# Performance work log

Hardware: AMD Instinct MI355X
Metric: run time of the kernel (lower is better)

Reference implementation:

```python
import jax, jax.numpy as jnp
import numpy as np

B = 65536
DIM = 256       # latent_dim
N_EMBED = 1024  # codebook size


def setup_inputs() -> dict:
    key = jax.random.key(0)
    kx, ke = jax.random.split(key)
    x = jax.random.normal(kx, (B, DIM), dtype=jnp.float32)
    # rosinality Quantize stores codebook as embed[dim, n_embed]
    embed = jax.random.normal(ke, (DIM, N_EMBED), dtype=jnp.float32)
    return {"x": x, "embed": embed}


def reference(x, embed):
    # dist[b, k] = ||x_b||^2 - 2 x_b . e_k + ||e_k||^2  (negated for argmax in
    # the original; equivalent to argmin of the distance)
    x_sq = jnp.sum(x * x, axis=1, keepdims=True)            # [B, 1]
    e_sq = jnp.sum(embed * embed, axis=0, keepdims=True)    # [1, K]
    dist = x_sq - 2.0 * (x @ embed) + e_sq                  # [B, K]
    embed_ind = jnp.argmin(dist, axis=1)                    # [B] int
    # codebook lookup: embed.T is [K, dim]
    quantize = jnp.take(embed.T, embed_ind, axis=0)         # [B, dim]
    # commitment loss term
    diff = jnp.mean(jnp.square(jax.lax.stop_gradient(quantize) - x))
    # straight-through estimator
    quantize_st = x + jax.lax.stop_gradient(quantize - x)
    return quantize_st, diff, embed_ind
```

## Files before the change

### kernel.cpp

```cpp
#include <hip/hip_runtime.h>

#define NROWSQ   65536
#define NDIM     256
#define NCB      1024
#define DIFF_OFF 16777216
#define IDX_OFF  16777217

#define MARGIN_A 0.35f
#define MARGIN_B 1.5e-3f
#define SCORE_SHIFT 384.0f

typedef __attribute__((ext_vector_type(8))) short s16x8;
typedef __attribute__((ext_vector_type(4))) float f32x4;

__device__ __forceinline__ unsigned short f2bf(float f) {
  union { float f; unsigned u; } v; v.f = f;
  return (unsigned short)((v.u + 0x7FFFu + ((v.u >> 16) & 1u)) >> 16);
}

__device__ __forceinline__ void gll16(const void* g, void* l) {
  __builtin_amdgcn_global_load_lds(
      (const __attribute__((address_space(1))) unsigned int*)g,
      (__attribute__((address_space(3))) unsigned int*)l, 16, 0, 0);
}

__device__ __forceinline__ void top2_update(float& v1, int& i1, float& v2, int& i2,
                                            float v, int col) {
  if (v > v1 || (v == v1 && col < i1)) { v2 = v1; i2 = i1; v1 = v; i1 = col; }
  else if (v > v2 || (v == v2 && col < i2)) { v2 = v; i2 = col; }
}
__device__ __forceinline__ void top2_merge(float& v1, int& i1, float& v2, int& i2,
                                           float ov1, int oi1, float ov2, int oi2) {
  if (ov1 > v1 || (ov1 == v1 && oi1 < i1)) {
    float nv2 = v1; int ni2 = i1;
    if (ov2 > nv2 || (ov2 == nv2 && oi2 < ni2)) { nv2 = ov2; ni2 = oi2; }
    v1 = ov1; i1 = oi1; v2 = nv2; i2 = ni2;
  } else if (ov1 > v2 || (ov1 == v2 && oi1 < i2)) {
    v2 = ov1; i2 = oi1;
  }
}

__device__ __forceinline__ float np_pairwise128(const float* p) {
  float r0 = p[0], r1 = p[1], r2 = p[2], r3 = p[3];
  float r4 = p[4], r5 = p[5], r6 = p[6], r7 = p[7];
  for (int i = 8; i < 128; i += 8) {
    r0 += p[i];     r1 += p[i + 1]; r2 += p[i + 2]; r3 += p[i + 3];
    r4 += p[i + 4]; r5 += p[i + 5]; r6 += p[i + 6]; r7 += p[i + 7];
  }
  return ((r0 + r1) + (r2 + r3)) + ((r4 + r5) + (r6 + r7));
}

__global__ void k0a_transpose(const float* __restrict__ E, float* __restrict__ embT,
                              unsigned short* __restrict__ cbT,
                              int* __restrict__ cntA, int* __restrict__ cntB) {
  __shared__ float T[64][65];
  const int t = threadIdx.x;
  const int kbase = (blockIdx.x & 15) * 64;
  const int dbase = (blockIdx.x >> 4) * 64;
  if (blockIdx.x == 0 && t == 0) { *cntA = 0; *cntB = 0; }
  #pragma unroll
  for (int i = 0; i < 4; ++i) {
    const int cid = i * 256 + t;
    const int dl = cid >> 4, kc = cid & 15;
    const float4 v = *(const float4*)(E + (size_t)(dbase + dl) * NCB + kbase + kc * 4);
    T[dl][kc * 4 + 0] = v.x; T[dl][kc * 4 + 1] = v.y;
    T[dl][kc * 4 + 2] = v.z; T[dl][kc * 4 + 3] = v.w;
  }
  __syncthreads();
  #pragma unroll
  for (int i = 0; i < 4; ++i) {
    const int cid = i * 256 + t;
    const int kl = cid >> 4, dc = cid & 15;
    float4 v;
    v.x = T[dc * 4 + 0][kl]; v.y = T[dc * 4 + 1][kl];
    v.z = T[dc * 4 + 2][kl]; v.w = T[dc * 4 + 3][kl];
    *(float4*)(embT + (size_t)(kbase + kl) * NDIM + dbase + dc * 4) = v;
    ushort4 b;
    b.x = f2bf(v.x); b.y = f2bf(v.y); b.z = f2bf(v.z); b.w = f2bf(v.w);
    const int dcol = dbase + dc * 4;
    const int sp = dcol ^ ((kl & 7) << 3);
    *(ushort4*)(cbT + (size_t)(kbase + kl) * NDIM + sp) = b;
  }
}

__global__ void k0b_esq(const float* __restrict__ embT, float* __restrict__ esq32,
                        float* __restrict__ esqs, float* __restrict__ esqr) {
  const int b = blockIdx.x, t = threadIdx.x;
  if (b < 128) {
    const int col = b * 8 + (t >> 5);
    const int l = t & 31;
    double s = 0.0;
    #pragma unroll
    for (int i = 0; i < 8; ++i) {
      const double v = (double)embT[(size_t)col * NDIM + l + i * 32];
      s += v * v;
    }
    #pragma unroll
    for (int m = 16; m >= 1; m >>= 1) s += __shfl_xor(s, m);
    if (l == 0) {
      esq32[col] = (float)(0.5 * s);
      esqs[col] = (float)(0.5 * s) - SCORE_SHIFT;
    }
  } else {
    __shared__ float Ls[16][260];
    const int col0 = (b - 128) * 16;
    #pragma unroll
    for (int i = 0; i < 4; ++i) {
      const int flat = i * 256 + t;
      const int row = flat >> 6, f4 = flat & 63;
      *(float4*)&Ls[row][f4 * 4] =
          *(const float4*)(embT + (size_t)(col0 + row) * NDIM + f4 * 4);
    }
    __syncthreads();
    if (t < 16) {
      float sr = 0.f;
      for (int d = 0; d < NDIM; ++d) {
        const float v = Ls[t][d];
        sr = sr + v * v;
      }
      esqr[col0 + t] = sr;
    }
  }
}

__global__ void k1_scores(
    const float* __restrict__ X, const unsigned short* __restrict__ cbT,
    const float* __restrict__ esqs, int2* __restrict__ part1) {
  __shared__ __align__(16) unsigned short Bs[2][64 * 256];
  __shared__ float esq_l[1024];
  const int t = threadIdx.x;
  const int lane = t & 63, w = t >> 6;
  const int l15 = lane & 15, quad = lane >> 4;
  const int rowbase = blockIdx.x * 128;
  const int swz = (l15 & 7) << 3;

  #pragma unroll
  for (int i = 0; i < 8; ++i)
    gll16(cbT + (size_t)(i * 256 + t) * 8, &Bs[0][(i * 256 + w * 64) * 8]);

  s16x8 afrag[2][8];
  #pragma unroll
  for (int m = 0; m < 2; ++m) {
    const float* xr = X + (size_t)(rowbase + w * 32 + m * 16 + l15) * NDIM;
    #pragma unroll
    for (int ks = 0; ks < 8; ++ks) {
      const float4 xa = *(const float4*)(xr + ks * 32 + quad * 8);
      const float4 xb = *(const float4*)(xr + ks * 32 + quad * 8 + 4);
      s16x8 a;
      a[0] = (short)f2bf(xa.x); a[1] = (short)f2bf(xa.y);
      a[2] = (short)f2bf(xa.z); a[3] = (short)f2bf(xa.w);
      a[4] = (short)f2bf(xb.x); a[5] = (short)f2bf(xb.y);
      a[6] = (short)f2bf(xb.z); a[7] = (short)f2bf(xb.w);
      afrag[m][ks] = a;
    }
  }

  {
    const float4 e4 = *(const float4*)(esqs + t * 4);
    *(float4*)(esq_l + t * 4) = e4;
  }

  int key1[2][4], key2[2][4];
  #pragma unroll
  for (int m = 0; m < 2; ++m)
    #pragma unroll
    for (int r = 0; r < 4; ++r) { key1[m][r] = 0; key2[m][r] = 0; }

  asm volatile("s_waitcnt vmcnt(0)" ::: "memory");
  __syncthreads();

  int cur = 0;
  for (int nt = 0; nt < 16; ++nt) {
    if (nt < 15) {
      const unsigned short* src = cbT + (size_t)(nt + 1) * (64 * 256);
      #pragma unroll
      for (int i = 0; i < 8; ++i)
        gll16(src + (size_t)(i * 256 + t) * 8, &Bs[cur ^ 1][(i * 256 + w * 64) * 8]);
    }

    f32x4 acc[2][4];
    #pragma unroll
    for (int m = 0; m < 2; ++m)
      #pragma unroll
      for (int s = 0; s < 4; ++s) acc[m][s] = (f32x4){0.f, 0.f, 0.f, 0.f};

    #pragma unroll
    for (int ks = 0; ks < 8; ++ks) {
      #pragma unroll
      for (int s = 0; s < 4; ++s) {
        const int us = (s * 16 + l15) * 256 + ((ks * 32 + quad * 8) ^ swz);
        const s16x8 bfr = *(const s16x8*)&Bs[cur][us];
        acc[0][s] = __builtin_amdgcn_mfma_f32_16x16x32_bf16(afrag[0][ks], bfr, acc[0][s], 0, 0, 0);
        acc[1][s] = __builtin_amdgcn_mfma_f32_16x16x32_bf16(afrag[1][ks], bfr, acc[1][s], 0, 0, 0);
      }
    }

    #pragma unroll
    for (int s = 0; s < 4; ++s) {
      const int lcol = nt * 64 + s * 16 + l15;
      const float eq = esq_l[lcol];
      const int suffix = 1023 - lcol;
      #pragma unroll
      for (int m = 0; m < 2; ++m)
        #pragma unroll
        for (int r = 0; r < 4; ++r) {
          float sc = acc[m][s][r] - eq;
          sc = fmaxf(sc, 1.0f);
          const int key = (__float_as_int(sc) & 0xFFFFFC00) | suffix;
          key2[m][r] = max(key2[m][r], min(key1[m][r], key));
          key1[m][r] = max(key1[m][r], key);
        }
    }

    asm volatile("s_waitcnt vmcnt(0)" ::: "memory");
    __syncthreads();
    cur ^= 1;
  }

  #pragma unroll
  for (int mask = 1; mask <= 8; mask <<= 1) {
    #pragma unroll
    for (int m = 0; m < 2; ++m)
      #pragma unroll
      for (int r = 0; r < 4; ++r) {
        const int ok1 = __shfl_xor(key1[m][r], mask);
        const int ok2 = __shfl_xor(key2[m][r], mask);
        const int n1 = max(key1[m][r], ok1);
        const int n2 = max(min(key1[m][r], ok1), max(key2[m][r], ok2));
        key1[m][r] = n1; key2[m][r] = n2;
      }
  }

  if (l15 == 0) {
    #pragma unroll
    for (int m = 0; m < 2; ++m)
      #pragma unroll
      for (int r = 0; r < 4; ++r) {
        const int grow = rowbase + w * 32 + m * 16 + quad * 4 + r;
        part1[grow] = make_int2(key1[m][r], key2[m][r]);
      }
  }
}

__global__ void k1m_merge(const int2* __restrict__ part1, float* __restrict__ outIdx,
                          int* __restrict__ cntA, int* __restrict__ listA,
                          float* __restrict__ outDiff) {
  const int row = blockIdx.x * 256 + threadIdx.x;
  if (row == 0) *outDiff = 0.f;
  const int2 a = part1[row];
  outIdx[row] = (float)(1023 - (a.x & 1023));
  const float g1 = __int_as_float(a.x & 0xFFFFFC00);
  const float g2 = __int_as_float(a.y & 0xFFFFFC00);
  if (g1 - g2 < MARGIN_A) {
    const int p = atomicAdd(cntA, 1);
    listA[p] = row;
  }
}

__global__ __launch_bounds__(256) void k2a_refine(
    const float* __restrict__ X, const float* __restrict__ E,
    const float* __restrict__ esq, const int* __restrict__ cntA,
    const int* __restrict__ listA, float4* __restrict__ part2) {
  __shared__ float Xs[8][NDIM];
  __shared__ float rv1[4][8], rv2[4][8];
  __shared__ int   ri1[4][8], ri2[4][8];
  const int t = threadIdx.x;
  const int lane = t & 63, w = t >> 6;
  const int half = blockIdx.x & 1;
  const int bstride = gridDim.x >> 1;
  const int cnt = *cntA;
  const int k0 = half * 512 + t * 2;
  for (int base = (blockIdx.x >> 1) * 8; base < cnt; base += bstride * 8) {
    const int nrows = min(8, cnt - base);
    __syncthreads();
    for (int r = 0; r < 8; ++r) {
      const int rid = listA[base + min(r, nrows - 1)];
      Xs[r][t] = X[(size_t)rid * NDIM + t];
    }
    __syncthreads();

    float acc[8][2];
    #pragma unroll
    for (int r = 0; r < 8; ++r) { acc[r][0] = 0.f; acc[r][1] = 0.f; }

    for (int d = 0; d < NDIM; ++d) {
      const float2 e = *(const float2*)(E + d * NCB + k0);
      #pragma unroll
      for (int r = 0; r < 8; ++r) {
        const float x = Xs[r][d];
        acc[r][0] += x * e.x; acc[r][1] += x * e.y;
      }
    }
    const float eq0 = esq[k0], eq1 = esq[k0 + 1];

    #pragma unroll
    for (int r = 0; r < 8; ++r) {
      float bv1 = -3.4e38f, bv2 = -3.4e38f; int bi1 = 0x7fffffff, bi2 = 0x7fffffff;
      top2_update(bv1, bi1, bv2, bi2, acc[r][0] - eq0, k0);
      top2_update(bv1, bi1, bv2, bi2, acc[r][1] - eq1, k0 + 1);
      #pragma unroll
      for (int mask = 1; mask < 64; mask <<= 1) {
        const float ov1 = __shfl_xor(bv1, mask); const int oi1 = __shfl_xor(bi1, mask);
        const float ov2 = __shfl_xor(bv2, mask); const int oi2 = __shfl_xor(bi2, mask);
        top2_merge(bv1, bi1, bv2, bi2, ov1, oi1, ov2, oi2);
      }
      if (lane == 0) { rv1[w][r] = bv1; ri1[w][r] = bi1; rv2[w][r] = bv2; ri2[w][r] = bi2; }
    }
    __syncthreads();
    if (t < nrows) {
      const int r = t;
      float fv1 = rv1[0][r], fv2 = rv2[0][r]; int fi1 = ri1[0][r], fi2 = ri2[0][r];
      for (int ww = 1; ww < 4; ++ww)
        top2_merge(fv1, fi1, fv2, fi2, rv1[ww][r], ri1[ww][r], rv2[ww][r], ri2[ww][r]);
      part2[half * NROWSQ + base + r] = make_float4(fv1, (float)fi1, fv2, (float)fi2);
    }
    __syncthreads();
  }
}

__global__ void k2m_merge(const float4* __restrict__ part2, const int* __restrict__ cntA,
                          const int* __restrict__ listA, float* __restrict__ outIdx,
                          int* __restrict__ cntB, int* __restrict__ listB) {
  const int cnt = *cntA;
  for (int j = blockIdx.x * 256 + threadIdx.x; j < cnt; j += gridDim.x * 256) {
    const float4 a = part2[j];
    const float4 b = part2[NROWSQ + j];
    float v1 = a.x, v2 = a.z; int i1 = (int)a.y, i2 = (int)a.w;
    top2_merge(v1, i1, v2, i2, b.x, (int)b.y, b.z, (int)b.w);
    const int rid = listA[j];
    outIdx[rid] = (float)i1;
    if (v1 - v2 < MARGIN_B) { const int p = atomicAdd(cntB, 1); listB[p] = rid; }
  }
}

__global__ __launch_bounds__(256) void k2b_mimic(
    const float* __restrict__ X, const float* __restrict__ embT,
    const float* __restrict__ esqr, const int* __restrict__ cntB,
    const int* __restrict__ listB, float* __restrict__ outIdx) {
  __shared__ float Xr[NDIM];
  __shared__ float Psq[NDIM];
  __shared__ float rv[256];
  __shared__ int ri[256];
  const int t = threadIdx.x;
  const int cnt = *cntB;
  for (int j = blockIdx.x; j < cnt; j += gridDim.x) {
    const int rid = listB[j];
    __syncthreads();
    {
      const float x = X[(size_t)rid * NDIM + t];
      Xr[t] = x;
      Psq[t] = x * x;
    }
    __syncthreads();
    const float x_sq = np_pairwise128(Psq) + np_pairwise128(Psq + 128);

    float best = 3.4e38f; int bidx = 0x7fffffff;
    #pragma unroll
    for (int c = 0; c < 4; ++c) {
      const int k = t + c * 256;
      const float* er = embT + (size_t)k * NDIM;
      float acc = 0.f;
      #pragma unroll 8
      for (int dq = 0; dq < 64; ++dq) {
        const float4 e = *(const float4*)(er + dq * 4);
        const float4 x = *(const float4*)(Xr + dq * 4);
        acc = fmaf(x.x, e.x, acc);
        acc = fmaf(x.y, e.y, acc);
        acc = fmaf(x.z, e.z, acc);
        acc = fmaf(x.w, e.w, acc);
      }
      const float dist = (x_sq - 2.0f * acc) + esqr[k];
      if (dist < best || (dist == best && k < bidx)) { best = dist; bidx = k; }
    }
    rv[t] = best; ri[t] = bidx;
    __syncthreads();
    for (int off = 128; off > 0; off >>= 1) {
      if (t < off) {
        if (rv[t + off] < rv[t] || (rv[t + off] == rv[t] && ri[t + off] < ri[t])) {
          rv[t] = rv[t + off]; ri[t] = ri[t + off];
        }
      }
      __syncthreads();
    }
    if (t == 0) outIdx[rid] = (float)ri[0];
  }
}

__global__ __launch_bounds__(256) void k4_outputs(
    const float* __restrict__ X, const float* __restrict__ embT,
    const float* __restrict__ idxF, float* __restrict__ outQ,
    float* __restrict__ outDiff) {
  const int t = threadIdx.x;
  const int lane = t & 63, w = t >> 6;
  const int W = blockIdx.x * 4 + w;
  float s = 0.f;
  #pragma unroll
  for (int i = 0; i < 8; ++i) {
    const int r = W + i * 8192;
    const int idx = (int)idxF[r];
    const float4 q = *(const float4*)(embT + idx * NDIM + lane * 4);
    const float4 x = *(const float4*)(X + (size_t)r * NDIM + lane * 4);
    *(float4*)(outQ + (size_t)r * NDIM + lane * 4) = q;
    const float dx = q.x - x.x, dy = q.y - x.y, dz = q.z - x.z, dw = q.w - x.w;
    s += dx * dx + dy * dy + dz * dz + dw * dw;
  }
  #pragma unroll
  for (int mask = 1; mask < 64; mask <<= 1) s += __shfl_xor(s, mask);
  __shared__ float bs[4];
  if (lane == 0) bs[w] = s;
  __syncthreads();
  if (t == 0)
    atomicAdd(outDiff, (bs[0] + bs[1] + bs[2] + bs[3]) * (1.0f / 16777216.0f));
}

extern "C" void kernel_launch(void* const* d_in, const int* in_sizes, int n_in,
                              void* d_out, int out_size, void* d_ws, size_t ws_size,
                              hipStream_t stream) {
  const float* X = (const float*)d_in[0];
  const float* E = (const float*)d_in[1];
  float* out = (float*)d_out;

  char* ws = (char*)d_ws;
  unsigned short* cbT = (unsigned short*)(ws + 0x000000);
  float*  embT  = (float*) (ws + 0x080000);
  float*  esq32 = (float*) (ws + 0x180000);
  float*  esqs  = (float*) (ws + 0x181000);
  float*  esqr  = (float*) (ws + 0x182000);
  int* cntA  = (int*)(ws + 0x183000);
  int* cntB  = (int*)(ws + 0x183004);
  int* listA = (int*)(ws + 0x183100);
  int* listB = (int*)(ws + 0x1C3100);
  int2*   part1 = (int2*)  (ws + 0x203100);
  float4* part2 = (float4*)(ws + 0x303100);

  float* outQ    = out;
  float* outDiff = out + DIFF_OFF;
  float* outIdx  = out + IDX_OFF;

  k0a_transpose<<<dim3(64), dim3(256), 0, stream>>>(E, embT, cbT, cntA, cntB);
  k0b_esq<<<dim3(192), dim3(256), 0, stream>>>(embT, esq32, esqs, esqr);
  k1_scores<<<dim3(512), dim3(256), 0, stream>>>(X, cbT, esqs, part1);
  k1m_merge<<<dim3(256), dim3(256), 0, stream>>>(part1, outIdx, cntA, listA, outDiff);
  k2a_refine<<<dim3(1024), dim3(256), 0, stream>>>(X, E, esq32, cntA, listA, part2);
  k2m_merge<<<dim3(64), dim3(256), 0, stream>>>(part2, cntA, listA, outIdx, cntB, listB);
  k2b_mimic<<<dim3(64), dim3(256), 0, stream>>>(X, embT, esqr, cntB, listB, outIdx);
  k4_outputs<<<dim3(2048), dim3(256), 0, stream>>>(X, embT, outIdx, outQ, outDiff);
}
```

Measured before the change: 319.4 us.

## Refine with transposed codebook rows and a four-way codebook split

The refine kernel now reads the transposed codebook so each thread walks one contiguous codebook row with float4 loads, and X rows are read from LDS as float4. The codebook is split across four blocks per row group instead of two, with one column per thread and a doubled grid. The merge kernel combines four partial top-2 results, and the partial buffer is relocated to hold four slices. In exchange, the per-thread row accesses are strided across lanes, X rows are loaded by more blocks, and the merge does more work.

```diff
diff --git a/kernel.cpp b/kernel.cpp
--- a/kernel.cpp
+++ b/kernel.cpp
@@ -258,19 +258,22 @@
 }
 
 __global__ __launch_bounds__(256) void k2a_refine(
-    const float* __restrict__ X, const float* __restrict__ E,
+    const float* __restrict__ X, const float* __restrict__ embT,
     const float* __restrict__ esq, const int* __restrict__ cntA,
     const int* __restrict__ listA, float4* __restrict__ part2) {
   __shared__ float Xs[8][NDIM];
-  __shared__ float rv1[4][8], rv2[4][8];
-  __shared__ int   ri1[4][8], ri2[4][8];
+  __shared__ float sv1[4][8], sv2[4][8];
+  __shared__ int   si1[4][8], si2[4][8];
   const int t = threadIdx.x;
   const int lane = t & 63, w = t >> 6;
-  const int half = blockIdx.x & 1;
-  const int bstride = gridDim.x >> 1;
+  const int split = blockIdx.x & 3;
+  const int col = split * 256 + t;
+  const int nslots = gridDim.x >> 2;
   const int cnt = *cntA;
-  const int k0 = half * 512 + t * 2;
-  for (int base = (blockIdx.x >> 1) * 8; base < cnt; base += bstride * 8) {
+  const float eqc = esq[col];
+  const float* er = embT + (size_t)col * NDIM;
+
+  for (int base = (blockIdx.x >> 2) * 8; base < cnt; base += nslots * 8) {
     const int nrows = min(8, cnt - base);
     __syncthreads();
     for (int r = 0; r < 8; ++r) {
@@ -279,40 +282,44 @@
     }
     __syncthreads();
 
-    float acc[8][2];
-    #pragma unroll
-    for (int r = 0; r < 8; ++r) { acc[r][0] = 0.f; acc[r][1] = 0.f; }
-
-    for (int d = 0; d < NDIM; ++d) {
-      const float2 e = *(const float2*)(E + d * NCB + k0);
+    float acc[8];
+    #pragma unroll
+    for (int r = 0; r < 8; ++r) acc[r] = 0.f;
+
+    #pragma unroll 4
+    for (int dq = 0; dq < 64; ++dq) {
+      const float4 e = *(const float4*)(er + dq * 4);
       #pragma unroll
       for (int r = 0; r < 8; ++r) {
-        const float x = Xs[r][d];
-        acc[r][0] += x * e.x; acc[r][1] += x * e.y;
-      }
-    }
-    const float eq0 = esq[k0], eq1 = esq[k0 + 1];
+        const float4 x = *(const float4*)(&Xs[r][dq * 4]);
+        float a = acc[r];
+        a = fmaf(x.x, e.x, a);
+        a = fmaf(x.y, e.y, a);
+        a = fmaf(x.z, e.z, a);
+        a = fmaf(x.w, e.w, a);
+        acc[r] = a;
+      }
+    }
 
     #pragma unroll
     for (int r = 0; r < 8; ++r) {
-      float bv1 = -3.4e38f, bv2 = -3.4e38f; int bi1 = 0x7fffffff, bi2 = 0x7fffffff;
-      top2_update(bv1, bi1, bv2, bi2, acc[r][0] - eq0, k0);
-      top2_update(bv1, bi1, bv2, bi2, acc[r][1] - eq1, k0 + 1);
+      float v1 = acc[r] - eqc, v2 = -3.4e38f;
+      int   i1 = col, i2 = 0x7fffffff;
       #pragma unroll
       for (int mask = 1; mask < 64; mask <<= 1) {
-        const float ov1 = __shfl_xor(bv1, mask); const int oi1 = __shfl_xor(bi1, mask);
-        const float ov2 = __shfl_xor(bv2, mask); const int oi2 = __shfl_xor(bi2, mask);
-        top2_merge(bv1, bi1, bv2, bi2, ov1, oi1, ov2, oi2);
-      }
-      if (lane == 0) { rv1[w][r] = bv1; ri1[w][r] = bi1; rv2[w][r] = bv2; ri2[w][r] = bi2; }
+        const float ov1 = __shfl_xor(v1, mask); const int oi1 = __shfl_xor(i1, mask);
+        const float ov2 = __shfl_xor(v2, mask); const int oi2 = __shfl_xor(i2, mask);
+        top2_merge(v1, i1, v2, i2, ov1, oi1, ov2, oi2);
+      }
+      if (lane == 0) { sv1[w][r] = v1; si1[w][r] = i1; sv2[w][r] = v2; si2[w][r] = i2; }
     }
     __syncthreads();
     if (t < nrows) {
       const int r = t;
-      float fv1 = rv1[0][r], fv2 = rv2[0][r]; int fi1 = ri1[0][r], fi2 = ri2[0][r];
+      float fv1 = sv1[0][r], fv2 = sv2[0][r]; int fi1 = si1[0][r], fi2 = si2[0][r];
       for (int ww = 1; ww < 4; ++ww)
-        top2_merge(fv1, fi1, fv2, fi2, rv1[ww][r], ri1[ww][r], rv2[ww][r], ri2[ww][r]);
-      part2[half * NROWSQ + base + r] = make_float4(fv1, (float)fi1, fv2, (float)fi2);
+        top2_merge(fv1, fi1, fv2, fi2, sv1[ww][r], si1[ww][r], sv2[ww][r], si2[ww][r]);
+      part2[(size_t)split * NROWSQ + base + r] = make_float4(fv1, (float)fi1, fv2, (float)fi2);
     }
     __syncthreads();
   }
@@ -324,9 +331,12 @@
   const int cnt = *cntA;
   for (int j = blockIdx.x * 256 + threadIdx.x; j < cnt; j += gridDim.x * 256) {
     const float4 a = part2[j];
-    const float4 b = part2[NROWSQ + j];
     float v1 = a.x, v2 = a.z; int i1 = (int)a.y, i2 = (int)a.w;
-    top2_merge(v1, i1, v2, i2, b.x, (int)b.y, b.z, (int)b.w);
+    #pragma unroll
+    for (int s = 1; s < 4; ++s) {
+      const float4 b = part2[(size_t)s * NROWSQ + j];
+      top2_merge(v1, i1, v2, i2, b.x, (int)b.y, b.z, (int)b.w);
+    }
     const int rid = listA[j];
     outIdx[rid] = (float)i1;
     if (v1 - v2 < MARGIN_B) { const int p = atomicAdd(cntB, 1); listB[p] = rid; }
@@ -431,7 +441,7 @@
   int* listA = (int*)(ws + 0x183100);
   int* listB = (int*)(ws + 0x1C3100);
   int2*   part1 = (int2*)  (ws + 0x203100);
-  float4* part2 = (float4*)(ws + 0x303100);
+  float4* part2 = (float4*)(ws + 0x283100);
 
   float* outQ    = out;
   float* outDiff = out + DIFF_OFF;
@@ -441,7 +451,7 @@
   k0b_esq<<<dim3(192), dim3(256), 0, stream>>>(embT, esq32, esqs, esqr);
   k1_scores<<<dim3(512), dim3(256), 0, stream>>>(X, cbT, esqs, part1);
   k1m_merge<<<dim3(256), dim3(256), 0, stream>>>(part1, outIdx, cntA, listA, outDiff);
-  k2a_refine<<<dim3(1024), dim3(256), 0, stream>>>(X, E, esq32, cntA, listA, part2);
+  k2a_refine<<<dim3(2048), dim3(256), 0, stream>>>(X, embT, esq32, cntA, listA, part2);
   k2m_merge<<<dim3(64), dim3(256), 0, stream>>>(part2, cntA, listA, outIdx, cntB, listB);
   k2b_mimic<<<dim3(64), dim3(256), 0, stream>>>(X, embT, esqr, cntB, listB, outIdx);
   k4_outputs<<<dim3(2048), dim3(256), 0, stream>>>(X, embT, outIdx, outQ, outDiff);
```

New measurement: 343.6 us. 1.08x slower.
